# Kernel tuning notes

Measured on AMD Instinct MI355X. Metric: run time of the kernel, lower is better.

The kernel has to match this reference:

```python
import jax, jax.numpy as jnp
import numpy as np

LOCAL_RADIUS = 5


def setup_inputs() -> dict:
    key = jax.random.key(0)
    k1, k2, k3 = jax.random.split(key, 3)
    B, K, C, H = 4, 4096, 256, 128
    x = jax.random.normal(k1, (B, K, C), dtype=jnp.float32)
    W1 = jax.random.normal(k2, (C, H), dtype=jnp.float32) * (1.0 / np.sqrt(C))
    b1 = jnp.zeros((H,), dtype=jnp.float32)
    W2 = jax.random.normal(k3, (H, 1), dtype=jnp.float32) * (1.0 / np.sqrt(H))
    b2 = jnp.zeros((1,), dtype=jnp.float32)
    return {"x": x, "W1": W1, "b1": b1, "W2": W2, "b2": b2}


def reference(x, W1, b1, W2, b2):
    # x: [B, k, C]. The MLP score for column j is independent of the row i,
    # so compute it once per token instead of per (i, window) as in the torch loop.
    B, k, C = x.shape
    s = (jnp.tanh(x @ W1 + b1) @ W2 + b2)[..., 0]  # [B, k]
    idx = jnp.arange(k)
    band = (jnp.abs(idx[:, None] - idx[None, :]) <= LOCAL_RADIUS)  # [k, k]
    # Outside the band the original leaves scores at 0.0 (not -inf), so
    # out-of-window positions still contribute exp(0)=1 to the softmax.
    scores = jnp.where(band[None, :, :], s[:, None, :], jnp.float32(0.0))  # [B, k, k]
    weights = jax.nn.softmax(scores, axis=-1)  # [B, k, k]
    weighted = jnp.einsum('bij,bjc->bic', weights, x)  # [B, k, C]
    return weighted, weights
```

## Files before the change

kernel.cpp:

```cpp
#include <hip/hip_runtime.h>
#include <math.h>

#define B_ 4
#define K_ 4096
#define C_ 256
#define H_ 128
#define RAD 5


__global__ __launch_bounds__(128) void score_kernel(
    const float* __restrict__ x, const float* __restrict__ W1,
    const float* __restrict__ b1, const float* __restrict__ W2,
    const float* __restrict__ b2, float* __restrict__ s_out)
{
    __shared__ float xs[C_];
    __shared__ float red[2];
    const int tid = threadIdx.x;
    const int token = blockIdx.x;
    const float* xrow = x + (size_t)token * C_;
    if (tid < 64) ((float4*)xs)[tid] = ((const float4*)xrow)[tid];
    __syncthreads();

    float acc = b1[tid];
    #pragma unroll 8
    for (int c = 0; c < C_; c += 4) {
        float4 xv = *(const float4*)&xs[c];
        acc = fmaf(xv.x, W1[(c + 0) * H_ + tid], acc);
        acc = fmaf(xv.y, W1[(c + 1) * H_ + tid], acc);
        acc = fmaf(xv.z, W1[(c + 2) * H_ + tid], acc);
        acc = fmaf(xv.w, W1[(c + 3) * H_ + tid], acc);
    }
    float p = tanhf(acc) * W2[tid];
    #pragma unroll
    for (int off = 32; off > 0; off >>= 1) p += __shfl_down(p, off);
    if ((tid & 63) == 0) red[tid >> 6] = p;
    __syncthreads();
    if (tid == 0) s_out[token] = red[0] + red[1] + b2[0];
}

__global__ __launch_bounds__(256) void colsum_partial(
    const float* __restrict__ x, float* __restrict__ partial)
{
    const int tid = threadIdx.x;
    const int blk = blockIdx.x;
    const int b = blk >> 5, chunk = blk & 31;
    const float* base = x + ((size_t)b * K_ + (size_t)chunk * 128) * C_ + tid;
    float acc = 0.f;
    for (int kk = 0; kk < 128; ++kk) acc += base[(size_t)kk * C_];
    partial[(size_t)blk * C_ + tid] = acc;
}

__global__ __launch_bounds__(256) void colsum_final(
    const float* __restrict__ partial, float* __restrict__ Ssum)
{
    const int tid = threadIdx.x;
    const int b = blockIdx.x;
    float acc = 0.f;
    #pragma unroll
    for (int chunk = 0; chunk < 32; ++chunk)
        acc += partial[(size_t)(b * 32 + chunk) * C_ + tid];
    Ssum[b * C_ + tid] = acc;
}

__global__ __launch_bounds__(256) void attn_kernel(
    const float* __restrict__ x, const float* __restrict__ s,
    const float* __restrict__ Ssum, float* __restrict__ out)
{
    const int tid = threadIdx.x;
    const int blk = blockIdx.x;
    const int b = blk >> 12;
    const int i = blk & (K_ - 1);

    __shared__ float wb[2 * RAD + 1];
    __shared__ float woff_s;
    __shared__ int j0_s, j1_s;

    if (tid == 0) {
        int j0 = i - RAD; if (j0 < 0) j0 = 0;
        int j1 = i + RAD; if (j1 > K_ - 1) j1 = K_ - 1;
        int nb = j1 - j0 + 1;
        float sv[2 * RAD + 1];
        float m = 0.f;
        const float* srow = s + b * K_;
        for (int jj = 0; jj < nb; ++jj) {
            float v = srow[j0 + jj];
            sv[jj] = v;
            m = fmaxf(m, v);
        }
        float e0 = expf(-m);
        float D = (float)(K_ - nb) * e0;
        for (int jj = 0; jj < nb; ++jj) { float e = expf(sv[jj] - m); sv[jj] = e; D += e; }
        float inv = 1.0f / D;
        for (int jj = 0; jj < nb; ++jj) wb[jj] = sv[jj] * inv;
        woff_s = e0 * inv;
        j0_s = j0; j1_s = j1;
    }
    __syncthreads();
    const float woff = woff_s;
    const int j0 = j0_s, j1 = j1_s;

    float* wrow = out + (size_t)B_ * K_ * C_ + (size_t)blk * K_;
    {
        const int jbase = tid * 16;
        const bool touches = (j1 >= jbase) && (j0 <= jbase + 15);
        if (!touches) {
            float4 v = make_float4(woff, woff, woff, woff);
            float4* p4 = (float4*)(wrow + jbase);
            p4[0] = v; p4[1] = v; p4[2] = v; p4[3] = v;
        } else {
            for (int q = 0; q < 16; ++q) {
                int j = jbase + q;
                wrow[j] = (j >= j0 && j <= j1) ? wb[j - j0] : woff;
            }
        }
    }

    {
        float acc = woff * Ssum[b * C_ + tid];
        const float* xb = x + ((size_t)b * K_) * C_ + tid;
        for (int j = j0; j <= j1; ++j)
            acc = fmaf(wb[j - j0] - woff, xb[(size_t)j * C_], acc);
        out[(size_t)blk * C_ + tid] = acc;
    }
}

extern "C" void kernel_launch(void* const* d_in, const int* in_sizes, int n_in,
                              void* d_out, int out_size, void* d_ws, size_t ws_size,
                              hipStream_t stream) {
    const float* x  = (const float*)d_in[0];
    const float* W1 = (const float*)d_in[1];
    const float* b1 = (const float*)d_in[2];
    const float* W2 = (const float*)d_in[3];
    const float* b2 = (const float*)d_in[4];
    float* out = (float*)d_out;

    float* ws      = (float*)d_ws;
    float* s       = ws;
    float* Ssum    = ws + B_ * K_;
    float* partial = Ssum + B_ * C_;

    score_kernel  <<<B_ * K_, 128, 0, stream>>>(x, W1, b1, W2, b2, s);
    colsum_partial<<<B_ * 32, 256, 0, stream>>>(x, partial);
    colsum_final  <<<B_,      256, 0, stream>>>(partial, Ssum);
    attn_kernel   <<<B_ * K_, 256, 0, stream>>>(x, s, Ssum, out);
}
```

Before: 427.6 us.

## Batch score tokens per block, widen colsum, use nontemporal vector stores

The score kernel now has each block handle 8 tokens, so every W1 weight load is reused across 8 rows instead of being reloaded per token. The column-sum partial kernel is split into 4x more blocks with 4 independent accumulators, and its scratch buffer moves into the weights region of the output, which is overwritten later. The attention kernel writes the dense weights row as coalesced float4 nontemporal stores, and the output rows also use nontemporal stores, to reduce cache pollution from the large write stream. In exchange, the score kernel holds more registers and reads x rows directly from global memory instead of staging them in shared memory.

```diff
diff --git a/kernel.cpp b/kernel.cpp
--- a/kernel.cpp
+++ b/kernel.cpp
@@ -7,35 +7,51 @@
 #define H_ 128
 #define RAD 5
 
+typedef float floatx4 __attribute__((ext_vector_type(4)));
+
 
 __global__ __launch_bounds__(128) void score_kernel(
     const float* __restrict__ x, const float* __restrict__ W1,
     const float* __restrict__ b1, const float* __restrict__ W2,
     const float* __restrict__ b2, float* __restrict__ s_out)
 {
-    __shared__ float xs[C_];
-    __shared__ float red[2];
     const int tid = threadIdx.x;
-    const int token = blockIdx.x;
-    const float* xrow = x + (size_t)token * C_;
-    if (tid < 64) ((float4*)xs)[tid] = ((const float4*)xrow)[tid];
+    const int t0 = blockIdx.x * 8;
+    const float* xr[8];
+    #pragma unroll
+    for (int t = 0; t < 8; ++t) xr[t] = x + (size_t)(t0 + t) * C_;
+
+    float acc[8];
+    float binit = b1[tid];
+    #pragma unroll
+    for (int t = 0; t < 8; ++t) acc[t] = binit;
+
+    for (int c = 0; c < C_; c += 4) {
+        float w0 = W1[(c + 0) * H_ + tid];
+        float w1 = W1[(c + 1) * H_ + tid];
+        float w2 = W1[(c + 2) * H_ + tid];
+        float w3 = W1[(c + 3) * H_ + tid];
+        #pragma unroll
+        for (int t = 0; t < 8; ++t) {
+            floatx4 xv = *(const floatx4*)&xr[t][c];
+            acc[t] = fmaf(xv.x, w0, acc[t]);
+            acc[t] = fmaf(xv.y, w1, acc[t]);
+            acc[t] = fmaf(xv.z, w2, acc[t]);
+            acc[t] = fmaf(xv.w, w3, acc[t]);
+        }
+    }
+
+    __shared__ float red[2][8];
+    float w2v = W2[tid];
+    #pragma unroll
+    for (int t = 0; t < 8; ++t) {
+        float p = tanhf(acc[t]) * w2v;
+        #pragma unroll
+        for (int off = 32; off > 0; off >>= 1) p += __shfl_down(p, off);
+        if ((tid & 63) == 0) red[tid >> 6][t] = p;
+    }
     __syncthreads();
-
-    float acc = b1[tid];
-    #pragma unroll 8
-    for (int c = 0; c < C_; c += 4) {
-        float4 xv = *(const float4*)&xs[c];
-        acc = fmaf(xv.x, W1[(c + 0) * H_ + tid], acc);
-        acc = fmaf(xv.y, W1[(c + 1) * H_ + tid], acc);
-        acc = fmaf(xv.z, W1[(c + 2) * H_ + tid], acc);
-        acc = fmaf(xv.w, W1[(c + 3) * H_ + tid], acc);
-    }
-    float p = tanhf(acc) * W2[tid];
-    #pragma unroll
-    for (int off = 32; off > 0; off >>= 1) p += __shfl_down(p, off);
-    if ((tid & 63) == 0) red[tid >> 6] = p;
-    __syncthreads();
-    if (tid == 0) s_out[token] = red[0] + red[1] + b2[0];
+    if (tid < 8) s_out[t0 + tid] = red[0][tid] + red[1][tid] + b2[0];
 }
 
 __global__ __launch_bounds__(256) void colsum_partial(
@@ -43,11 +59,16 @@
 {
     const int tid = threadIdx.x;
     const int blk = blockIdx.x;
-    const int b = blk >> 5, chunk = blk & 31;
-    const float* base = x + ((size_t)b * K_ + (size_t)chunk * 128) * C_ + tid;
-    float acc = 0.f;
-    for (int kk = 0; kk < 128; ++kk) acc += base[(size_t)kk * C_];
-    partial[(size_t)blk * C_ + tid] = acc;
+    const float* base = x + (size_t)blk * 32 * C_ + tid;
+    float a0 = 0.f, a1 = 0.f, a2 = 0.f, a3 = 0.f;
+    #pragma unroll
+    for (int kk = 0; kk < 32; kk += 4) {
+        a0 += base[(size_t)(kk + 0) * C_];
+        a1 += base[(size_t)(kk + 1) * C_];
+        a2 += base[(size_t)(kk + 2) * C_];
+        a3 += base[(size_t)(kk + 3) * C_];
+    }
+    partial[(size_t)blk * C_ + tid] = (a0 + a1) + (a2 + a3);
 }
 
 __global__ __launch_bounds__(256) void colsum_final(
@@ -56,9 +77,8 @@
     const int tid = threadIdx.x;
     const int b = blockIdx.x;
     float acc = 0.f;
-    #pragma unroll
-    for (int chunk = 0; chunk < 32; ++chunk)
-        acc += partial[(size_t)(b * 32 + chunk) * C_ + tid];
+    for (int chunk = 0; chunk < 128; ++chunk)
+        acc += partial[(size_t)(b * 128 + chunk) * C_ + tid];
     Ssum[b * C_ + tid] = acc;
 }
 
@@ -99,20 +119,19 @@
     const float woff = woff_s;
     const int j0 = j0_s, j1 = j1_s;
 
-    float* wrow = out + (size_t)B_ * K_ * C_ + (size_t)blk * K_;
-    {
-        const int jbase = tid * 16;
-        const bool touches = (j1 >= jbase) && (j0 <= jbase + 15);
-        if (!touches) {
-            float4 v = make_float4(woff, woff, woff, woff);
-            float4* p4 = (float4*)(wrow + jbase);
-            p4[0] = v; p4[1] = v; p4[2] = v; p4[3] = v;
-        } else {
-            for (int q = 0; q < 16; ++q) {
-                int j = jbase + q;
-                wrow[j] = (j >= j0 && j <= j1) ? wb[j - j0] : woff;
-            }
+    floatx4* wrow4 = (floatx4*)(out + (size_t)B_ * K_ * C_ + (size_t)blk * K_);
+    #pragma unroll
+    for (int q = 0; q < 4; ++q) {
+        const int f = tid + 256 * q;
+        const int jb = f * 4;
+        floatx4 v = { woff, woff, woff, woff };
+        if (jb + 3 >= j0 && jb <= j1) {
+            if (jb + 0 >= j0 && jb + 0 <= j1) v.x = wb[jb + 0 - j0];
+            if (jb + 1 >= j0 && jb + 1 <= j1) v.y = wb[jb + 1 - j0];
+            if (jb + 2 >= j0 && jb + 2 <= j1) v.z = wb[jb + 2 - j0];
+            if (jb + 3 >= j0 && jb + 3 <= j1) v.w = wb[jb + 3 - j0];
         }
+        __builtin_nontemporal_store(v, wrow4 + f);
     }
 
     {
@@ -120,7 +139,7 @@
         const float* xb = x + ((size_t)b * K_) * C_ + tid;
         for (int j = j0; j <= j1; ++j)
             acc = fmaf(wb[j - j0] - woff, xb[(size_t)j * C_], acc);
-        out[(size_t)blk * C_ + tid] = acc;
+        __builtin_nontemporal_store(acc, out + (size_t)blk * C_ + tid);
     }
 }
 
@@ -134,13 +153,13 @@
     const float* b2 = (const float*)d_in[4];
     float* out = (float*)d_out;
 
-    float* ws      = (float*)d_ws;
-    float* s       = ws;
-    float* Ssum    = ws + B_ * K_;
-    float* partial = Ssum + B_ * C_;
+    float* ws   = (float*)d_ws;
+    float* s    = ws;
+    float* Ssum = ws + B_ * K_;
+    float* partial = out + (size_t)B_ * K_ * C_;
 
-    score_kernel  <<<B_ * K_, 128, 0, stream>>>(x, W1, b1, W2, b2, s);
-    colsum_partial<<<B_ * 32, 256, 0, stream>>>(x, partial);
-    colsum_final  <<<B_,      256, 0, stream>>>(partial, Ssum);
-    attn_kernel   <<<B_ * K_, 256, 0, stream>>>(x, s, Ssum, out);
+    score_kernel  <<<B_ * K_ / 8, 128, 0, stream>>>(x, W1, b1, W2, b2, s);
+    colsum_partial<<<B_ * 128,    256, 0, stream>>>(x, partial);
+    colsum_final  <<<B_,          256, 0, stream>>>(partial, Ssum);
+    attn_kernel   <<<B_ * K_,     256, 0, stream>>>(x, s, Ssum, out);
 }
```

Measured after the change: 390.9 us. 1.09x faster.
